# Kernel optimization log

Hardware: AMD Instinct MI355X
Metric: run time of the kernel (lower is better)

## Reference

```python
import jax, jax.numpy as jnp
import numpy as np

# ---------- static mesh topology helpers (numpy, setup-time only) ----------

def _topo_subdivide(nv, faces):
    edge_id = {}
    mids = []
    nf = []
    def mid(a, b):
        k = (a, b) if a < b else (b, a)
        if k not in edge_id:
            edge_id[k] = nv + len(mids)
            mids.append(k)
        return edge_id[k]
    for a, b, c in faces:
        a, b, c = int(a), int(b), int(c)
        ab, bc, ca = mid(a, b), mid(b, c), mid(c, a)
        nf += [[a, ab, ca], [b, bc, ab], [c, ca, bc], [ab, bc, ca]]
    return np.array(nf, dtype=np.int64), np.array(mids, dtype=np.int64)

def _icosphere(level, radius):
    t = (1.0 + 5.0 ** 0.5) / 2.0
    v = np.array([[-1, t, 0], [1, t, 0], [-1, -t, 0], [1, -t, 0],
                  [0, -1, t], [0, 1, t], [0, -1, -t], [0, 1, -t],
                  [t, 0, -1], [t, 0, 1], [-t, 0, -1], [-t, 0, 1]], dtype=np.float64)
    v /= np.linalg.norm(v, axis=1, keepdims=True)
    f = np.array([[0, 11, 5], [0, 5, 1], [0, 1, 7], [0, 7, 10], [0, 10, 11],
                  [1, 5, 9], [5, 11, 4], [11, 10, 2], [10, 7, 6], [7, 1, 8],
                  [3, 9, 4], [3, 4, 2], [3, 2, 6], [3, 6, 8], [3, 8, 9],
                  [4, 9, 5], [2, 4, 11], [6, 2, 10], [8, 6, 7], [9, 8, 1]], dtype=np.int64)
    for _ in range(level):
        f, mids = _topo_subdivide(len(v), f)
        mv = v[mids[:, 0]] + v[mids[:, 1]]
        mv /= np.linalg.norm(mv, axis=1, keepdims=True)
        v = np.concatenate([v, mv], 0)
    return (v * radius).astype(np.float32), f

def _directed_edges(faces):
    e = np.concatenate([faces[:, [0, 1]], faces[:, [1, 2]], faces[:, [2, 0]],
                        faces[:, [1, 0]], faces[:, [2, 1]], faces[:, [0, 2]]], 0)
    return np.unique(e, axis=0).T.astype(np.int64)  # (2, E) directed, deduped

# ---------- jax forward math ----------

def _project(verts, camera_c, camera_f):
    # K @ [I | t], t = (0,0,0.8): rows [f0,0,c0,0.8*c0],[0,f1,c1,0.8*c1],[0,0,1,0.8]
    z = jnp.zeros((), verts.dtype); o = jnp.ones((), verts.dtype)
    tz = jnp.asarray(0.8, verts.dtype)
    P = jnp.stack([
        jnp.stack([camera_f[0], z, camera_c[0], tz * camera_c[0]]),
        jnp.stack([z, camera_f[1], camera_c[1], tz * camera_c[1]]),
        jnp.stack([z, z, o, tz])])
    hom = jnp.concatenate([verts, jnp.ones((verts.shape[0], 1), verts.dtype)], 1)
    pc = hom @ P.T                     # (V, 3)
    return pc[:, :2] / pc[:, 2:3]      # (V, 2) pixel coords [x, y]

def _bilerp(feat, px, py, image_size):
    # feat: (C, dim, dim); px, py: (V,)
    dim = feat.shape[1]
    x = px * dim / image_size
    y = py * dim / image_size
    x1 = jnp.floor(x); x2 = x1 + 1.0
    y1 = jnp.floor(y); y2 = y1 + 1.0
    xi1 = jnp.clip(x1.astype(jnp.int32), 0, dim - 1)
    xi2 = jnp.clip(x2.astype(jnp.int32), 0, dim - 1)
    yi1 = jnp.clip(y1.astype(jnp.int32), 0, dim - 1)
    yi2 = jnp.clip(y2.astype(jnp.int32), 0, dim - 1)
    f11 = feat[:, xi1, yi1].T  # (V, C)
    f12 = feat[:, xi1, yi2].T
    f21 = feat[:, xi2, yi1].T
    f22 = feat[:, xi2, yi2].T
    w11 = ((x2 - x) * (y2 - y))[:, None]
    w12 = ((x2 - x) * (y - y1))[:, None]
    w21 = ((x - x1) * (y2 - y))[:, None]
    w22 = ((x - x1) * (y - y1))[:, None]
    return w11 * f11 + w12 * f12 + w21 * f21 + w22 * f22

def _gconv(x, W0, W1, b, src, dst):
    agg = jax.ops.segment_sum(x[dst], src, num_segments=x.shape[0])
    return x @ W0 + agg @ W1 + b

def _gresnet(x, edges, params):
    Win0, Win1, bin_, W0s, W1s, bs, Wc0, Wc1, bc = params
    src, dst = edges[0], edges[1]
    h = jax.nn.relu(_gconv(x, Win0, Win1, bin_, src, dst))
    def body(h, lw):
        W0, W1, b = lw
        return jax.nn.relu(_gconv(h, W0, W1, b, src, dst)) + h, None
    h, _ = jax.lax.scan(body, h, (W0s, W1s, bs))
    coords = _gconv(h, Wc0, Wc1, bc, src, dst)
    return h, coords

def _forward(f3, f4, f5, verts0, camera_c, camera_f, p1, p2, p3,
             edges1, edges2, edges3, mid0, mid1, image_size):
    def deform(verts, shape_feat, edges, params):
        pix = _project(verts, camera_c, camera_f)
        px, py = pix[:, 0], pix[:, 1]
        perc = jnp.concatenate([_bilerp(f3, px, py, image_size),
                                _bilerp(f4, px, py, image_size),
                                _bilerp(f5, px, py, image_size)], 1)  # (V, 1280)
        feats = jnp.concatenate([perc, shape_feat], 1)
        h, coords = _gresnet(feats, edges, params)
        return coords, h
    def unpool(verts, feat, mid):
        vf = jnp.concatenate([verts, feat], 1)
        new = (vf[mid[:, 0]] + vf[mid[:, 1]]) * 0.5  # edge midpoints
        vf = jnp.concatenate([vf, new], 0)
        return vf[:, :3], vf[:, 3:]
    verts, feat = deform(verts0, verts0, edges1, p1)
    verts, feat = unpool(verts, feat, mid0)
    verts, feat = deform(verts, feat, edges2, p2)
    verts, feat = unpool(verts, feat, mid1)
    verts, _ = deform(verts, feat, edges3, p3)
    return verts  # (40962, 3)

# ---------- harness entry points ----------

def setup_inputs() -> dict:
    key = jax.random.key(0)
    keys = iter(jax.random.split(key, 64))
    v0, f0 = _icosphere(4, 0.2)                      # 2562 verts, 5120 faces
    f1, mid0 = _topo_subdivide(len(v0), f0)          # -> 10242 verts topology
    f2, mid1 = _topo_subdivide(len(v0) + len(mid0), f1)  # -> 40962 verts
    inp = {
        'f3': jax.random.normal(next(keys), (256, 56, 56), jnp.float32),
        'f4': jax.random.normal(next(keys), (512, 28, 28), jnp.float32),
        'f5': jax.random.normal(next(keys), (512, 14, 14), jnp.float32),
        'verts0': jnp.asarray(v0),
        'camera_c': jnp.array([112.0, 112.0], jnp.float32),
        'camera_f': jnp.array([248.0, 248.0], jnp.float32),
    }
    D, L = 128, 12
    def stage(prefix, in_dim):
        def w(shape, scale):
            return jax.random.normal(next(keys), shape, jnp.float32) * scale
        inp[prefix + '_Win0'] = w((in_dim, D), 1.0 / np.sqrt(in_dim))
        inp[prefix + '_Win1'] = w((in_dim, D), 1.0 / np.sqrt(in_dim))
        inp[prefix + '_bin'] = jnp.zeros((D,), jnp.float32)
        inp[prefix + '_W0'] = w((L, D, D), 0.3 / np.sqrt(D))
        inp[prefix + '_W1'] = w((L, D, D), 0.3 / np.sqrt(D))
        inp[prefix + '_b'] = jnp.zeros((L, D), jnp.float32)
        inp[prefix + '_Wc0'] = w((D, 3), 0.01 / np.sqrt(D))
        inp[prefix + '_Wc1'] = w((D, 3), 0.01 / np.sqrt(D))
        inp[prefix + '_bc'] = jnp.zeros((3,), jnp.float32)
    stage('g1', 1283)
    stage('g2', 1408)
    stage('g3', 1408)
    inp['edges1'] = jnp.asarray(_directed_edges(f0))   # (2, 15360)
    inp['edges2'] = jnp.asarray(_directed_edges(f1))   # (2, 61440)
    inp['edges3'] = jnp.asarray(_directed_edges(f2))   # (2, 245760)
    inp['mid0'] = jnp.asarray(mid0)                    # (7680, 2)
    inp['mid1'] = jnp.asarray(mid1)                    # (30720, 2)
    inp['image_size'] = 224
    return inp

def reference(f3, f4, f5, verts0, camera_c, camera_f,
              g1_Win0, g1_Win1, g1_bin, g1_W0, g1_W1, g1_b, g1_Wc0, g1_Wc1, g1_bc,
              g2_Win0, g2_Win1, g2_bin, g2_W0, g2_W1, g2_b, g2_Wc0, g2_Wc1, g2_bc,
              g3_Win0, g3_Win1, g3_bin, g3_W0, g3_W1, g3_b, g3_Wc0, g3_Wc1, g3_bc,
              edges1, edges2, edges3, mid0, mid1, image_size):
    p1 = (g1_Win0, g1_Win1, g1_bin, g1_W0, g1_W1, g1_b, g1_Wc0, g1_Wc1, g1_bc)
    p2 = (g2_Win0, g2_Win1, g2_bin, g2_W0, g2_W1, g2_b, g2_Wc0, g2_Wc1, g2_bc)
    p3 = (g3_Win0, g3_Win1, g3_bin, g3_W0, g3_W1, g3_b, g3_Wc0, g3_Wc1, g3_bc)
    return _forward(f3, f4, f5, verts0, camera_c, camera_f, p1, p2, p3,
                    edges1, edges2, edges3, mid0, mid1, image_size)
```

## Files before the change

### kernel.cpp

```cpp
#include <hip/hip_runtime.h>
#include <hip/hip_bf16.h>
#include <cstddef>
#include <cstdint>

#define DIV_UP(a, b) (((a) + (b) - 1) / (b))

typedef __attribute__((ext_vector_type(8))) short bf16x8v;
typedef __attribute__((ext_vector_type(4))) float f32x4v;

__device__ __forceinline__ unsigned short bf16_rn(float v) {
    unsigned int u = __float_as_uint(v);
    unsigned int r = (u + 0x7FFFu + ((u >> 16) & 1u)) >> 16;
    return (unsigned short)r;
}
__device__ __forceinline__ float bf16_f(unsigned short h) {
    return __uint_as_float(((unsigned int)h) << 16);
}
__device__ __forceinline__ void f2hl(float v, unsigned short& hi, unsigned short& lo) {
    hi = bf16_rn(v);
    float r = v - bf16_f(hi);
    lo = bf16_rn(r);
}

__global__ void transpose_hl(const float* __restrict__ in, unsigned short* __restrict__ ohi,
                             unsigned short* __restrict__ olo, int C, int HW) {
    int idx = blockIdx.x * 256 + threadIdx.x;
    if (idx >= C * HW) return;
    int c = idx % C;
    int p = idx / C;
    float v = in[(size_t)c * HW + p];
    unsigned short hi, lo;
    f2hl(v, hi, lo);
    ohi[(size_t)p * C + c] = hi;
    olo[(size_t)p * C + c] = lo;
}

__global__ void pack_gb_bt(const float* __restrict__ W00, const float* __restrict__ W01,
                           const float* __restrict__ W10, const float* __restrict__ W11,
                           const float* __restrict__ W20, const float* __restrict__ W21,
                           unsigned short* __restrict__ Bhi, unsigned short* __restrict__ Blo,
                           int base, int C) {
    int idx = blockIdx.x * 256 + threadIdx.x;
    if (idx >= 768 * C) return;
    int n = idx / C, k = idx % C;
    int s = n >> 8, j = n & 255;
    const float* W0 = (s == 0) ? W00 : (s == 1) ? W10 : W20;
    const float* W1 = (s == 0) ? W01 : (s == 1) ? W11 : W21;
    float v = (j < 128) ? W0[(size_t)(base + k) * 128 + j]
                        : W1[(size_t)(base + k) * 128 + (j - 128)];
    unsigned short hi, lo;
    f2hl(v, hi, lo);
    Bhi[idx] = hi;
    Blo[idx] = lo;
}

__global__ void pack_lay_bt(const float* __restrict__ W0, const float* __restrict__ W1,
                            unsigned short* __restrict__ Bhi, unsigned short* __restrict__ Blo) {
    int idx = blockIdx.x * 256 + threadIdx.x;
    int l = idx >> 15;
    int r = idx & 32767;
    int n = r >> 8, k = r & 255;
    float v = (k < 128) ? W0[(size_t)l * 16384 + k * 128 + n]
                        : W1[(size_t)l * 16384 + (k - 128) * 128 + n];
    unsigned short hi, lo;
    f2hl(v, hi, lo);
    Bhi[idx] = hi;
    Blo[idx] = lo;
}

__global__ void pack_sh_bt(const float* __restrict__ Win0, const float* __restrict__ Win1,
                           unsigned short* __restrict__ Bhi, unsigned short* __restrict__ Blo) {
    int idx = blockIdx.x * 256 + threadIdx.x;
    if (idx >= 256 * 128) return;
    int n = idx >> 7, k = idx & 127;
    float v = (n < 128) ? Win0[(size_t)(1280 + k) * 128 + n]
                        : Win1[(size_t)(1280 + k) * 128 + (n - 128)];
    unsigned short hi, lo;
    f2hl(v, hi, lo);
    Bhi[idx] = hi;
    Blo[idx] = lo;
}

__global__ void desc_kernel(const float* __restrict__ verts,
                            const float* __restrict__ cam_c, const float* __restrict__ cam_f,
                            const int* __restrict__ imgsz, int V,
                            int* __restrict__ sampi, float* __restrict__ sampw) {
    int v = blockIdx.x * 256 + threadIdx.x;
    if (v >= V) return;
    float X = verts[3 * v + 0], Yy = verts[3 * v + 1], Z = verts[3 * v + 2];
    float cx = cam_c[0], cy = cam_c[1], fx = cam_f[0], fy = cam_f[1];
    const float tz = 0.8f;
    float pz = Z + tz;
    float px = (fx * X + cx * Z + tz * cx) / pz;
    float py = (fy * Yy + cy * Z + tz * cy) / pz;
    float is = (float)imgsz[0];
    const int Ss[3] = {56, 28, 14};
#pragma unroll
    for (int m = 0; m < 3; ++m) {
        int S = Ss[m];
        float dim = (float)S;
        float x = px * dim / is;
        float y = py * dim / is;
        float x1 = floorf(x), y1 = floorf(y);
        float x2 = x1 + 1.0f, y2 = y1 + 1.0f;
        float smax = (float)(S - 1);
        int xi1 = (int)fminf(fmaxf(x1, 0.0f), smax);
        int xi2 = (int)fminf(fmaxf(x2, 0.0f), smax);
        int yi1 = (int)fminf(fmaxf(y1, 0.0f), smax);
        int yi2 = (int)fminf(fmaxf(y2, 0.0f), smax);
        int b = v * 12 + m * 4;
        sampi[b + 0] = xi1 * S + yi1;
        sampi[b + 1] = xi1 * S + yi2;
        sampi[b + 2] = xi2 * S + yi1;
        sampi[b + 3] = xi2 * S + yi2;
        sampw[b + 0] = (x2 - x) * (y2 - y);
        sampw[b + 1] = (x2 - x) * (y - y1);
        sampw[b + 2] = (x - x1) * (y2 - y);
        sampw[b + 3] = (x - x1) * (y - y1);
    }
}

__global__ void rowptr_kernel(const int* __restrict__ src, int E, int V, int* __restrict__ rowptr) {
    int v = blockIdx.x * 256 + threadIdx.x;
    if (v > V) return;
    int lo = 0, hi = E;
    while (lo < hi) {
        int mid = (lo + hi) >> 1;
        if (src[mid] < v) lo = mid + 1; else hi = mid;
    }
    rowptr[v] = lo;
}

struct MArgs {
    const unsigned short *Ahi, *Alo; int lda;
    const unsigned short *Bhi, *Blo; int K;
    float* Y;
    int sstr;
    int V;
};

template <int EPI>
__global__ __launch_bounds__(256) void mgemm(MArgs g) {
    __shared__ unsigned short As_hi[64][40], As_lo[64][40];
    __shared__ unsigned short Bs_hi[128][40], Bs_lo[128][40];
    int tid = threadIdx.x;
    int row0 = blockIdx.y * 64;
    int col0 = blockIdx.x * 128;
    int l = tid & 63, wid = tid >> 6;
    int wr = wid & 1, wc = wid >> 1;
    int lw = l & 15, gg = l >> 4;
    f32x4v acc[2][4];
#pragma unroll
    for (int i = 0; i < 2; ++i)
#pragma unroll
        for (int j = 0; j < 4; ++j) acc[i][j] = (f32x4v){0.f, 0.f, 0.f, 0.f};

    int arow = tid >> 2, akoff = (tid & 3) * 8;
    for (int k0 = 0; k0 < g.K; k0 += 32) {
        __syncthreads();
        {
            int grow = row0 + arow;
            uint4 zh = make_uint4(0, 0, 0, 0), zl = make_uint4(0, 0, 0, 0);
            if (grow < g.V) {
                zh = *(const uint4*)(g.Ahi + (size_t)grow * g.lda + k0 + akoff);
                zl = *(const uint4*)(g.Alo + (size_t)grow * g.lda + k0 + akoff);
            }
            *(uint4*)&As_hi[arow][akoff] = zh;
            *(uint4*)&As_lo[arow][akoff] = zl;
        }
#pragma unroll
        for (int it = 0; it < 2; ++it) {
            int q = tid + it * 256;
            int n = q >> 2, koff = (q & 3) * 8;
            *(uint4*)&Bs_hi[n][koff] = *(const uint4*)(g.Bhi + (size_t)(col0 + n) * g.K + k0 + koff);
            *(uint4*)&Bs_lo[n][koff] = *(const uint4*)(g.Blo + (size_t)(col0 + n) * g.K + k0 + koff);
        }
        __syncthreads();
        bf16x8v ah[2], al[2], bh[4], bl[4];
#pragma unroll
        for (int mt = 0; mt < 2; ++mt) {
            int r = wr * 32 + mt * 16 + lw;
            ah[mt] = *(const bf16x8v*)&As_hi[r][gg * 8];
            al[mt] = *(const bf16x8v*)&As_lo[r][gg * 8];
        }
#pragma unroll
        for (int nt = 0; nt < 4; ++nt) {
            int c = wc * 64 + nt * 16 + lw;
            bh[nt] = *(const bf16x8v*)&Bs_hi[c][gg * 8];
            bl[nt] = *(const bf16x8v*)&Bs_lo[c][gg * 8];
        }
#pragma unroll
        for (int mt = 0; mt < 2; ++mt)
#pragma unroll
            for (int nt = 0; nt < 4; ++nt) {
                acc[mt][nt] = __builtin_amdgcn_mfma_f32_16x16x32_bf16(ah[mt], bh[nt], acc[mt][nt], 0, 0, 0);
                acc[mt][nt] = __builtin_amdgcn_mfma_f32_16x16x32_bf16(ah[mt], bl[nt], acc[mt][nt], 0, 0, 0);
                acc[mt][nt] = __builtin_amdgcn_mfma_f32_16x16x32_bf16(al[mt], bh[nt], acc[mt][nt], 0, 0, 0);
            }
    }
#pragma unroll
    for (int mt = 0; mt < 2; ++mt)
#pragma unroll
        for (int nt = 0; nt < 4; ++nt) {
            int colg = wc * 64 + nt * 16 + lw;
#pragma unroll
            for (int r = 0; r < 4; ++r) {
                int rowg = row0 + wr * 32 + mt * 16 + gg * 4 + r;
                if (rowg >= g.V) continue;
                float v = acc[mt][nt][r];
                if (EPI == 0) {
                    g.Y[(size_t)rowg * 256 + col0 + colg] += v;
                } else {
                    int cg = col0 + colg;
                    g.Y[(size_t)(cg >> 8) * g.sstr + (size_t)rowg * 256 + (cg & 255)] = v;
                }
            }
        }
}

__global__ void gather_kernel(const float* __restrict__ G, int sstr,
                              const int* __restrict__ sampi, const float* __restrict__ sampw,
                              float* __restrict__ Yb, int V, int stage,
                              const float* __restrict__ Win0, const float* __restrict__ Win1,
                              const float* __restrict__ shape) {
    int v = blockIdx.x;
    if (v >= V) return;
    int j = threadIdx.x;
    const float* Gs = G + (size_t)stage * sstr;
    int b = v * 12;
    float acc = 0.0f;
#pragma unroll
    for (int s = 0; s < 4; ++s)
        acc += sampw[b + s] * Gs[(size_t)sampi[b + s] * 256 + j];
#pragma unroll
    for (int s = 0; s < 4; ++s)
        acc += sampw[b + 4 + s] * Gs[(size_t)(3136 + sampi[b + 4 + s]) * 256 + j];
#pragma unroll
    for (int s = 0; s < 4; ++s)
        acc += sampw[b + 8 + s] * Gs[(size_t)(3920 + sampi[b + 8 + s]) * 256 + j];
    if (stage == 0) {
#pragma unroll
        for (int k = 0; k < 3; ++k) {
            float w = shape[v * 3 + k];
            float wv = (j < 128) ? Win0[(size_t)(1280 + k) * 128 + j]
                                 : Win1[(size_t)(1280 + k) * 128 + (j - 128)];
            acc += w * wv;
        }
    }
    Yb[(size_t)v * 256 + j] = acc;
}

__global__ __launch_bounds__(256) void combine_in(
    const float* __restrict__ Y, const float* __restrict__ bias,
    const int* __restrict__ rowptr, const int* __restrict__ dst,
    float* __restrict__ hout, int V) {
    int v = blockIdx.x * 2 + (threadIdx.x >> 7);
    int d = threadIdx.x & 127;
    if (v >= V) return;
    float val = Y[(size_t)v * 256 + d] + bias[d];
    int e0 = rowptr[v], e1 = rowptr[v + 1];
    for (int e = e0; e < e1; ++e) val += Y[(size_t)dst[e] * 256 + 128 + d];
    val = fmaxf(val, 0.0f);
    hout[(size_t)v * 128 + d] = val;
}

struct LArgs {
    const float* h;
    const unsigned short *Bhi, *Blo;
    const int *rowptr, *dst;
    const float* bias;
    float* hnext;
    int V;
};

__global__ __launch_bounds__(256) void lay_kernel(LArgs g) {
    __shared__ unsigned short As_hi[64][136], As_lo[64][136];
    __shared__ unsigned short Bs_hi[128][40], Bs_lo[128][40];
    int tid = threadIdx.x;
    int row0 = blockIdx.x * 64;
    int l = tid & 63, wid = tid >> 6;
    int wr = wid & 1, wc = wid >> 1;
    int lw = l & 15, gg = l >> 4;
    int arow = tid >> 2;
    int acq = (tid & 3) * 32;
    int grow = row0 + arow;

    f32x4v acc[2][4];
#pragma unroll
    for (int i = 0; i < 2; ++i)
#pragma unroll
        for (int j = 0; j < 4; ++j) acc[i][j] = (f32x4v){0.f, 0.f, 0.f, 0.f};

    float vals[32];

    auto store_half = [&]() {
        unsigned short hh[8], ll[8];
#pragma unroll
        for (int c = 0; c < 4; ++c) {
#pragma unroll
            for (int i = 0; i < 8; ++i) f2hl(vals[c * 8 + i], hh[i], ll[i]);
            *(uint4*)&As_hi[arow][acq + c * 8] = *(uint4*)hh;
            *(uint4*)&As_lo[arow][acq + c * 8] = *(uint4*)ll;
        }
    };

    auto mfma_step = [&](int ks, int kglob0) {
#pragma unroll
        for (int it = 0; it < 2; ++it) {
            int q = tid + it * 256;
            int n = q >> 2, koff = (q & 3) * 8;
            *(uint4*)&Bs_hi[n][koff] = *(const uint4*)(g.Bhi + (size_t)n * 256 + kglob0 + koff);
            *(uint4*)&Bs_lo[n][koff] = *(const uint4*)(g.Blo + (size_t)n * 256 + kglob0 + koff);
        }
        __syncthreads();
        bf16x8v ah[2], al[2], bh[4], bl[4];
        int kk = ks * 32 + gg * 8;
#pragma unroll
        for (int mt = 0; mt < 2; ++mt) {
            int r = wr * 32 + mt * 16 + lw;
            ah[mt] = *(const bf16x8v*)&As_hi[r][kk];
            al[mt] = *(const bf16x8v*)&As_lo[r][kk];
        }
#pragma unroll
        for (int nt = 0; nt < 4; ++nt) {
            int c = wc * 64 + nt * 16 + lw;
            bh[nt] = *(const bf16x8v*)&Bs_hi[c][gg * 8];
            bl[nt] = *(const bf16x8v*)&Bs_lo[c][gg * 8];
        }
#pragma unroll
        for (int mt = 0; mt < 2; ++mt)
#pragma unroll
            for (int nt = 0; nt < 4; ++nt) {
                acc[mt][nt] = __builtin_amdgcn_mfma_f32_16x16x32_bf16(ah[mt], bh[nt], acc[mt][nt], 0, 0, 0);
                acc[mt][nt] = __builtin_amdgcn_mfma_f32_16x16x32_bf16(ah[mt], bl[nt], acc[mt][nt], 0, 0, 0);
                acc[mt][nt] = __builtin_amdgcn_mfma_f32_16x16x32_bf16(al[mt], bh[nt], acc[mt][nt], 0, 0, 0);
            }
        __syncthreads();
    };

#pragma unroll
    for (int i = 0; i < 32; ++i) vals[i] = 0.0f;
    if (grow < g.V) {
        int e0 = g.rowptr[grow], e1 = g.rowptr[grow + 1];
        for (int e = e0; e < e1; ++e) {
            const float* hp = g.h + (size_t)g.dst[e] * 128 + acq;
#pragma unroll
            for (int c = 0; c < 8; ++c) {
                float4 f = *(const float4*)(hp + c * 4);
                vals[c * 4 + 0] += f.x;
                vals[c * 4 + 1] += f.y;
                vals[c * 4 + 2] += f.z;
                vals[c * 4 + 3] += f.w;
            }
        }
    }
    store_half();
    for (int ks = 0; ks < 4; ++ks) mfma_step(ks, 128 + ks * 32);

    if (grow < g.V) {
        const float* hp = g.h + (size_t)grow * 128 + acq;
#pragma unroll
        for (int c = 0; c < 8; ++c) {
            float4 f = *(const float4*)(hp + c * 4);
            vals[c * 4 + 0] = f.x;
            vals[c * 4 + 1] = f.y;
            vals[c * 4 + 2] = f.z;
            vals[c * 4 + 3] = f.w;
        }
    } else {
#pragma unroll
        for (int i = 0; i < 32; ++i) vals[i] = 0.0f;
    }
    store_half();
    for (int ks = 0; ks < 4; ++ks) mfma_step(ks, ks * 32);

#pragma unroll
    for (int mt = 0; mt < 2; ++mt)
#pragma unroll
        for (int nt = 0; nt < 4; ++nt) {
            int colg = wc * 64 + nt * 16 + lw;
            float bv = g.bias[colg];
#pragma unroll
            for (int r = 0; r < 4; ++r) {
                int rowg = row0 + wr * 32 + mt * 16 + gg * 4 + r;
                if (rowg >= g.V) continue;
                float v = acc[mt][nt][r] + bv;
                v = fmaxf(v, 0.0f);
                v += g.h[(size_t)rowg * 128 + colg];
                g.hnext[(size_t)rowg * 128 + colg] = v;
            }
        }
}

__global__ void coordgemm_kernel(const float* __restrict__ h,
                                 const float* __restrict__ Wc0, const float* __restrict__ Wc1,
                                 int V, float* __restrict__ Yc) {
    int idx = blockIdx.x * 256 + threadIdx.x;
    if (idx >= V * 6) return;
    int v = idx / 6, j = idx % 6;
    const float* W = (j < 3) ? Wc0 : Wc1;
    int jj = (j < 3) ? j : j - 3;
    const float* hp = h + (size_t)v * 128;
    float acc = 0.0f;
#pragma unroll 8
    for (int k = 0; k < 128; ++k) acc += hp[k] * W[k * 3 + jj];
    Yc[idx] = acc;
}

__global__ void coordcombine_kernel(const float* __restrict__ Yc, const float* __restrict__ bc,
                                    const int* __restrict__ rowptr, const int* __restrict__ dst,
                                    int V, float* __restrict__ out) {
    int idx = blockIdx.x * 256 + threadIdx.x;
    if (idx >= V * 3) return;
    int v = idx / 3, j = idx % 3;
    float val = Yc[(size_t)v * 6 + j] + bc[j];
    int e0 = rowptr[v], e1 = rowptr[v + 1];
    for (int e = e0; e < e1; ++e) val += Yc[(size_t)dst[e] * 6 + 3 + j];
    out[(size_t)v * 3 + j] = val;
}

__global__ void unpool_kernel(float* __restrict__ verts, const float* __restrict__ h,
                              const int* __restrict__ mid, int V, int Nm,
                              unsigned short* __restrict__ fphi, unsigned short* __restrict__ fplo) {
    int r = blockIdx.x;
    int t = threadIdx.x;
    if (r < V) {
        float v = h[(size_t)r * 128 + t];
        unsigned short hi, lo;
        f2hl(v, hi, lo);
        fphi[(size_t)r * 128 + t] = hi;
        fplo[(size_t)r * 128 + t] = lo;
    } else {
        int i = r - V;
        int a = mid[2 * i], b = mid[2 * i + 1];
        float v = 0.5f * (h[(size_t)a * 128 + t] + h[(size_t)b * 128 + t]);
        unsigned short hi, lo;
        f2hl(v, hi, lo);
        fphi[(size_t)r * 128 + t] = hi;
        fplo[(size_t)r * 128 + t] = lo;
        if (t < 3)
            verts[(size_t)r * 3 + t] = 0.5f * (verts[(size_t)a * 3 + t] + verts[(size_t)b * 3 + t]);
    }
}

extern "C" void kernel_launch(void* const* d_in, const int* in_sizes, int n_in,
                              void* d_out, int out_size, void* d_ws, size_t ws_size,
                              hipStream_t stream) {
    const float* f3 = (const float*)d_in[0];
    const float* f4 = (const float*)d_in[1];
    const float* f5 = (const float*)d_in[2];
    const float* verts0 = (const float*)d_in[3];
    const float* cam_c = (const float*)d_in[4];
    const float* cam_f = (const float*)d_in[5];
    const int* imgsz = (const int*)d_in[38];

    int V0 = in_sizes[3] / 3;
    int E[3] = {in_sizes[33] / 2, in_sizes[34] / 2, in_sizes[35] / 2};
    int Nm0 = in_sizes[36] / 2, Nm1 = in_sizes[37] / 2;
    int V1 = V0 + Nm0, V2 = V1 + Nm1;
    int Vs[3] = {V0, V1, V2};
    const int NPIXT = 3136 + 784 + 196;
    const int GS = NPIXT * 256;

    char* wsp = (char*)d_ws;
    auto alloc = [&](size_t bytes) -> void* {
        void* p = (void*)wsp;
        wsp += (bytes + 255) & ~(size_t)255;
        return p;
    };
    unsigned short* ft0h = (unsigned short*)alloc((size_t)3136 * 256 * 2);
    unsigned short* ft0l = (unsigned short*)alloc((size_t)3136 * 256 * 2);
    unsigned short* ft1h = (unsigned short*)alloc((size_t)784 * 512 * 2);
    unsigned short* ft1l = (unsigned short*)alloc((size_t)784 * 512 * 2);
    unsigned short* ft2h = (unsigned short*)alloc((size_t)196 * 512 * 2);
    unsigned short* ft2l = (unsigned short*)alloc((size_t)196 * 512 * 2);
    unsigned short* Bg0h = (unsigned short*)alloc((size_t)768 * 256 * 2);
    unsigned short* Bg0l = (unsigned short*)alloc((size_t)768 * 256 * 2);
    unsigned short* Bg1h = (unsigned short*)alloc((size_t)768 * 512 * 2);
    unsigned short* Bg1l = (unsigned short*)alloc((size_t)768 * 512 * 2);
    unsigned short* Bg2h = (unsigned short*)alloc((size_t)768 * 512 * 2);
    unsigned short* Bg2l = (unsigned short*)alloc((size_t)768 * 512 * 2);
    float* Gbuf = (float*)alloc((size_t)3 * GS * 4);
    unsigned short* BtLhi = (unsigned short*)alloc((size_t)12 * 128 * 256 * 2);
    unsigned short* BtLlo = (unsigned short*)alloc((size_t)12 * 128 * 256 * 2);
    unsigned short* BtShi = (unsigned short*)alloc((size_t)256 * 128 * 2);
    unsigned short* BtSlo = (unsigned short*)alloc((size_t)256 * 128 * 2);
    float* Ybuf = (float*)alloc((size_t)V2 * 256 * 4);
    float* hA = (float*)alloc((size_t)V2 * 128 * 4);
    float* hB = (float*)alloc((size_t)V2 * 128 * 4);
    unsigned short* FPhi = (unsigned short*)alloc((size_t)V2 * 128 * 2);
    unsigned short* FPlo = (unsigned short*)alloc((size_t)V2 * 128 * 2);
    float* vertsbuf = (float*)alloc((size_t)V2 * 3 * 4);
    float* Yc = (float*)alloc((size_t)V2 * 6 * 4);
    int* sampi = (int*)alloc((size_t)V2 * 12 * 4);
    float* sampw = (float*)alloc((size_t)V2 * 12 * 4);
    int* rowptr = (int*)alloc(((size_t)V2 + 1) * 4);

    transpose_hl<<<DIV_UP(256 * 56 * 56, 256), 256, 0, stream>>>(f3, ft0h, ft0l, 256, 56 * 56);
    transpose_hl<<<DIV_UP(512 * 28 * 28, 256), 256, 0, stream>>>(f4, ft1h, ft1l, 512, 28 * 28);
    transpose_hl<<<DIV_UP(512 * 14 * 14, 256), 256, 0, stream>>>(f5, ft2h, ft2l, 512, 14 * 14);

    const float* W0s_[3] = {(const float*)d_in[6], (const float*)d_in[15], (const float*)d_in[24]};
    const float* W1s_[3] = {(const float*)d_in[7], (const float*)d_in[16], (const float*)d_in[25]};

    pack_gb_bt<<<DIV_UP(768 * 256, 256), 256, 0, stream>>>(W0s_[0], W1s_[0], W0s_[1], W1s_[1],
                                                           W0s_[2], W1s_[2], Bg0h, Bg0l, 0, 256);
    pack_gb_bt<<<DIV_UP(768 * 512, 256), 256, 0, stream>>>(W0s_[0], W1s_[0], W0s_[1], W1s_[1],
                                                           W0s_[2], W1s_[2], Bg1h, Bg1l, 256, 512);
    pack_gb_bt<<<DIV_UP(768 * 512, 256), 256, 0, stream>>>(W0s_[0], W1s_[0], W0s_[1], W1s_[1],
                                                           W0s_[2], W1s_[2], Bg2h, Bg2l, 768, 512);
    {
        MArgs m = {};
        m.sstr = GS;
        m.Ahi = ft0h; m.Alo = ft0l; m.lda = 256;
        m.Bhi = Bg0h; m.Blo = Bg0l; m.K = 256;
        m.Y = Gbuf; m.V = 3136;
        dim3 g0(6, DIV_UP(3136, 64));
        mgemm<2><<<g0, 256, 0, stream>>>(m);
        m.Ahi = ft1h; m.Alo = ft1l; m.lda = 512;
        m.Bhi = Bg1h; m.Blo = Bg1l; m.K = 512;
        m.Y = Gbuf + (size_t)3136 * 256; m.V = 784;
        dim3 g1(6, DIV_UP(784, 64));
        mgemm<2><<<g1, 256, 0, stream>>>(m);
        m.Ahi = ft2h; m.Alo = ft2l; m.lda = 512;
        m.Bhi = Bg2h; m.Blo = Bg2l; m.K = 512;
        m.Y = Gbuf + (size_t)3920 * 256; m.V = 196;
        dim3 g2(6, DIV_UP(196, 64));
        mgemm<2><<<g2, 256, 0, stream>>>(m);
    }

    for (int si = 0; si < 3; ++si) {
        const float* Win0 = (const float*)d_in[6 + si * 9 + 0];
        const float* Win1 = (const float*)d_in[6 + si * 9 + 1];
        const float* bin = (const float*)d_in[6 + si * 9 + 2];
        const float* W0L = (const float*)d_in[6 + si * 9 + 3];
        const float* W1L = (const float*)d_in[6 + si * 9 + 4];
        const float* bs = (const float*)d_in[6 + si * 9 + 5];
        const float* Wc0 = (const float*)d_in[6 + si * 9 + 6];
        const float* Wc1 = (const float*)d_in[6 + si * 9 + 7];
        const float* bc = (const float*)d_in[6 + si * 9 + 8];
        const int* edges = (const int*)d_in[33 + si];
        int Ecur = E[si];
        const int* esrc = edges;
        const int* edst = edges + Ecur;
        int V = Vs[si];
        const float* vertsin = (si == 0) ? verts0 : vertsbuf;

        pack_lay_bt<<<12 * 128, 256, 0, stream>>>(W0L, W1L, BtLhi, BtLlo);
        if (si > 0) pack_sh_bt<<<128, 256, 0, stream>>>(Win0, Win1, BtShi, BtSlo);
        desc_kernel<<<DIV_UP(V, 256), 256, 0, stream>>>(vertsin, cam_c, cam_f, imgsz, V,
                                                        sampi, sampw);
        rowptr_kernel<<<DIV_UP(V + 1, 256), 256, 0, stream>>>(esrc, Ecur, V, rowptr);

        gather_kernel<<<V, 256, 0, stream>>>(Gbuf, GS, sampi, sampw, Ybuf, V, si, Win0, Win1,
                                             (si == 0) ? verts0 : nullptr);
        if (si > 0) {
            MArgs m = {};
            m.Ahi = FPhi; m.Alo = FPlo; m.lda = 128;
            m.Bhi = BtShi; m.Blo = BtSlo; m.K = 128;
            m.Y = Ybuf; m.V = V;
            dim3 grid(2, DIV_UP(V, 64));
            mgemm<0><<<grid, 256, 0, stream>>>(m);
        }
        combine_in<<<DIV_UP(V, 2), 256, 0, stream>>>(Ybuf, bin, rowptr, edst, hA, V);

        float* hcur = hA;
        float* hnext = hB;
        for (int ll = 0; ll < 12; ++ll) {
            LArgs a = {};
            a.h = hcur;
            a.Bhi = BtLhi + (size_t)ll * 32768;
            a.Blo = BtLlo + (size_t)ll * 32768;
            a.rowptr = rowptr; a.dst = edst;
            a.bias = bs + (size_t)ll * 128;
            a.hnext = hnext;
            a.V = V;
            lay_kernel<<<DIV_UP(V, 64), 256, 0, stream>>>(a);
            float* t = hcur; hcur = hnext; hnext = t;
        }

        coordgemm_kernel<<<DIV_UP(V * 6, 256), 256, 0, stream>>>(hcur, Wc0, Wc1, V, Yc);
        float* ctarget = (si == 2) ? (float*)d_out : vertsbuf;
        coordcombine_kernel<<<DIV_UP(V * 3, 256), 256, 0, stream>>>(Yc, bc, rowptr, edst, V,
                                                                    ctarget);
        if (si < 2) {
            const int* mid = (const int*)d_in[36 + si];
            int Nm = (si == 0) ? Nm0 : Nm1;
            unpool_kernel<<<V + Nm, 128, 0, stream>>>(vertsbuf, hcur, mid, V, Nm, FPhi, FPlo);
        }
    }
}
```

Measured before the change: 1.530 ms.

## Shrink lay_kernel A tile, stage A per K-slice, remap blocks across XCDs

The A tile in shared memory shrinks from 64x128 to a 64x32 slice. Each K step now has only the owning thread quarter convert its 32 values to hi/lo bf16 and write them, which cuts LDS use and may allow higher occupancy. B-tile global loads are issued into registers before the A stores so they overlap, and workgroup IDs are remapped so consecutive row tiles land on the same XCD for L2 locality. The self-term GEMM now runs before the neighbour aggregation, and coordgemm reads h with float4 loads. The tradeoff is that only a quarter of threads do the conversion work in each step.

```diff
diff --git a/kernel.cpp b/kernel.cpp
--- a/kernel.cpp
+++ b/kernel.cpp
@@ -274,15 +274,22 @@
 };
 
 __global__ __launch_bounds__(256) void lay_kernel(LArgs g) {
-    __shared__ unsigned short As_hi[64][136], As_lo[64][136];
+    __shared__ unsigned short As_hi[64][40], As_lo[64][40];
     __shared__ unsigned short Bs_hi[128][40], Bs_lo[128][40];
     int tid = threadIdx.x;
-    int row0 = blockIdx.x * 64;
+
+    int nwg = gridDim.x;
+    int orig = blockIdx.x;
+    int qq = nwg >> 3, rr = nwg & 7;
+    int xcd = orig & 7, idx = orig >> 3;
+    int bid = (xcd < rr ? xcd * (qq + 1) : rr * (qq + 1) + (xcd - rr) * qq) + idx;
+    int row0 = bid * 64;
+
     int l = tid & 63, wid = tid >> 6;
     int wr = wid & 1, wc = wid >> 1;
     int lw = l & 15, gg = l >> 4;
     int arow = tid >> 2;
-    int acq = (tid & 3) * 32;
+    int aq = tid & 3;
     int grow = row0 + arow;
 
     f32x4v acc[2][4];
@@ -293,33 +300,40 @@
 
     float vals[32];
 
-    auto store_half = [&]() {
-        unsigned short hh[8], ll[8];
-#pragma unroll
-        for (int c = 0; c < 4; ++c) {
-#pragma unroll
-            for (int i = 0; i < 8; ++i) f2hl(vals[c * 8 + i], hh[i], ll[i]);
-            *(uint4*)&As_hi[arow][acq + c * 8] = *(uint4*)hh;
-            *(uint4*)&As_lo[arow][acq + c * 8] = *(uint4*)ll;
-        }
-    };
-
     auto mfma_step = [&](int ks, int kglob0) {
-#pragma unroll
-        for (int it = 0; it < 2; ++it) {
-            int q = tid + it * 256;
-            int n = q >> 2, koff = (q & 3) * 8;
-            *(uint4*)&Bs_hi[n][koff] = *(const uint4*)(g.Bhi + (size_t)n * 256 + kglob0 + koff);
-            *(uint4*)&Bs_lo[n][koff] = *(const uint4*)(g.Blo + (size_t)n * 256 + kglob0 + koff);
+        uint4 b0h, b1h, b0l, b1l;
+        {
+            int n0 = tid >> 2, koff = (tid & 3) * 8;
+            b0h = *(const uint4*)(g.Bhi + (size_t)n0 * 256 + kglob0 + koff);
+            b0l = *(const uint4*)(g.Blo + (size_t)n0 * 256 + kglob0 + koff);
+            int n1 = n0 + 64;
+            b1h = *(const uint4*)(g.Bhi + (size_t)n1 * 256 + kglob0 + koff);
+            b1l = *(const uint4*)(g.Blo + (size_t)n1 * 256 + kglob0 + koff);
+        }
+        if (aq == ks) {
+            unsigned short hh[8], ll[8];
+#pragma unroll
+            for (int c = 0; c < 4; ++c) {
+#pragma unroll
+                for (int i = 0; i < 8; ++i) f2hl(vals[c * 8 + i], hh[i], ll[i]);
+                *(uint4*)&As_hi[arow][c * 8] = *(uint4*)hh;
+                *(uint4*)&As_lo[arow][c * 8] = *(uint4*)ll;
+            }
+        }
+        {
+            int n0 = tid >> 2, koff = (tid & 3) * 8;
+            *(uint4*)&Bs_hi[n0][koff] = b0h;
+            *(uint4*)&Bs_lo[n0][koff] = b0l;
+            *(uint4*)&Bs_hi[n0 + 64][koff] = b1h;
+            *(uint4*)&Bs_lo[n0 + 64][koff] = b1l;
         }
         __syncthreads();
         bf16x8v ah[2], al[2], bh[4], bl[4];
-        int kk = ks * 32 + gg * 8;
 #pragma unroll
         for (int mt = 0; mt < 2; ++mt) {
             int r = wr * 32 + mt * 16 + lw;
-            ah[mt] = *(const bf16x8v*)&As_hi[r][kk];
-            al[mt] = *(const bf16x8v*)&As_lo[r][kk];
+            ah[mt] = *(const bf16x8v*)&As_hi[r][gg * 8];
+            al[mt] = *(const bf16x8v*)&As_lo[r][gg * 8];
         }
 #pragma unroll
         for (int nt = 0; nt < 4; ++nt) {
@@ -338,12 +352,28 @@
         __syncthreads();
     };
 
+    if (grow < g.V) {
+        const float* hp = g.h + (size_t)grow * 128 + aq * 32;
+#pragma unroll
+        for (int c = 0; c < 8; ++c) {
+            float4 f = *(const float4*)(hp + c * 4);
+            vals[c * 4 + 0] = f.x;
+            vals[c * 4 + 1] = f.y;
+            vals[c * 4 + 2] = f.z;
+            vals[c * 4 + 3] = f.w;
+        }
+    } else {
+#pragma unroll
+        for (int i = 0; i < 32; ++i) vals[i] = 0.0f;
+    }
+    for (int ks = 0; ks < 4; ++ks) mfma_step(ks, ks * 32);
+
 #pragma unroll
     for (int i = 0; i < 32; ++i) vals[i] = 0.0f;
     if (grow < g.V) {
         int e0 = g.rowptr[grow], e1 = g.rowptr[grow + 1];
         for (int e = e0; e < e1; ++e) {
-            const float* hp = g.h + (size_t)g.dst[e] * 128 + acq;
+            const float* hp = g.h + (size_t)g.dst[e] * 128 + aq * 32;
 #pragma unroll
             for (int c = 0; c < 8; ++c) {
                 float4 f = *(const float4*)(hp + c * 4);
@@ -354,25 +384,7 @@
             }
         }
     }
-    store_half();
     for (int ks = 0; ks < 4; ++ks) mfma_step(ks, 128 + ks * 32);
-
-    if (grow < g.V) {
-        const float* hp = g.h + (size_t)grow * 128 + acq;
-#pragma unroll
-        for (int c = 0; c < 8; ++c) {
-            float4 f = *(const float4*)(hp + c * 4);
-            vals[c * 4 + 0] = f.x;
-            vals[c * 4 + 1] = f.y;
-            vals[c * 4 + 2] = f.z;
-            vals[c * 4 + 3] = f.w;
-        }
-    } else {
-#pragma unroll
-        for (int i = 0; i < 32; ++i) vals[i] = 0.0f;
-    }
-    store_half();
-    for (int ks = 0; ks < 4; ++ks) mfma_step(ks, ks * 32);
 
 #pragma unroll
     for (int mt = 0; mt < 2; ++mt)
@@ -402,8 +414,14 @@
     int jj = (j < 3) ? j : j - 3;
     const float* hp = h + (size_t)v * 128;
     float acc = 0.0f;
-#pragma unroll 8
-    for (int k = 0; k < 128; ++k) acc += hp[k] * W[k * 3 + jj];
+#pragma unroll
+    for (int k = 0; k < 32; ++k) {
+        float4 f = *(const float4*)(hp + k * 4);
+        acc += f.x * W[(k * 4 + 0) * 3 + jj];
+        acc += f.y * W[(k * 4 + 1) * 3 + jj];
+        acc += f.z * W[(k * 4 + 2) * 3 + jj];
+        acc += f.w * W[(k * 4 + 3) * 3 + jj];
+    }
     Yc[idx] = acc;
 }
 
```

Result: no change. 1.511 ms (-1.2%).
